# Optimization experiments

Hardware: AMD Instinct MI355X
Metric: run time of the kernel (lower is better)

## Reference

```python
import jax, jax.numpy as jnp
import numpy as np

IN_FEATURES = 4096
OUT_FEATURES = 2048
N_GROUPS = 16  # group size = IN_FEATURES // N_GROUPS = 256


def setup_inputs() -> dict:
    key = jax.random.key(0)
    k1, k2, k3, k4 = jax.random.split(key, 4)
    x = jax.random.normal(k1, (8, 64, IN_FEATURES), dtype=jnp.float32)
    # uint8 quantized weights, stored [out, in] as in the torch module
    qweight = jax.random.randint(k2, (OUT_FEATURES, IN_FEATURES), 0, 256).astype(jnp.uint8)
    # per-(out-channel, group) dequant scale and offset; scale ~ (max-min)/255 of rand weights
    qrange = jax.random.uniform(k3, (OUT_FEATURES, N_GROUPS), dtype=jnp.float32) * (2.0 / 255.0)
    qmin = -jax.random.uniform(k4, (OUT_FEATURES, N_GROUPS), dtype=jnp.float32)
    return {"x": x, "qweight": qweight, "qrange": qrange, "qmin": qmin}


def reference(x, qweight, qrange, qmin):
    # out[b,s,o] = sum_i x[b,s,i] * (q[o,i]*qrange[o,g(i)] + qmin[o,g(i)])
    B, S, IN = x.shape
    OUT, G = qrange.shape
    gs = IN // G
    xg = x.reshape(B, S, G, gs)                     # [B,S,G,gs]
    qg = qweight.reshape(OUT, G, gs).astype(x.dtype)  # [O,G,gs]
    # fused per-group dequant matmul: scale folded into the contraction
    out = jnp.einsum('bsgi,ogi,og->bso', xg, qg, qrange)
    # offset term: qmin[o,g] * sum_i_in_group x[b,s,i]
    out = out + jnp.einsum('bsg,og->bso', xg.sum(axis=-1), qmin)
    return out
```

## Files before the change

kernel.cpp:

```cpp
#include <hip/hip_runtime.h>
#include <hip/hip_bf16.h>


#define M_T 512
#define N_T 2048
#define K_T 4096
#define NGRP 16
#define BM 128
#define BN 128
#define BK 64
#define OUT_ELEMS (M_T * N_T)
#define W_ELEMS (N_T * K_T)
#define X_ELEMS (M_T * K_T)

typedef __attribute__((ext_vector_type(8))) short mfrag_t;
typedef __attribute__((ext_vector_type(8))) unsigned short u16x8;
typedef __attribute__((ext_vector_type(4))) float f32x4;

__device__ __forceinline__ unsigned short f2bf(float f) {
  union { __hip_bfloat16 h; unsigned short u; } c;
  c.h = __float2bfloat16(f);
  return c.u;
}

__global__ __launch_bounds__(256) void pack_kernel(
    const float* __restrict__ x, const int* __restrict__ qw,
    const float* __restrict__ qrange, const float* __restrict__ qmin,
    unsigned short* __restrict__ wsW, unsigned short* __restrict__ wsX) {
  const int bid = blockIdx.x;
  const int tid = threadIdx.x;
  if (bid < (W_ELEMS / 8) / 256) {
    const int gidx = bid * 256 + tid;
    const int o = gidx >> 9;
    const int k8 = gidx & 511;
    const int g = k8 >> 5;
    const float sc = qrange[o * NGRP + g];
    const float mn = qmin[o * NGRP + g];
    const int4* q = (const int4*)(qw + ((size_t)o << 12) + (k8 << 3));
    const int4 q0 = q[0], q1 = q[1];
    u16x8 p;
    p[0] = f2bf((float)q0.x * sc + mn); p[1] = f2bf((float)q0.y * sc + mn);
    p[2] = f2bf((float)q0.z * sc + mn); p[3] = f2bf((float)q0.w * sc + mn);
    p[4] = f2bf((float)q1.x * sc + mn); p[5] = f2bf((float)q1.y * sc + mn);
    p[6] = f2bf((float)q1.z * sc + mn); p[7] = f2bf((float)q1.w * sc + mn);
    *(u16x8*)(wsW + ((size_t)gidx << 3)) = p;
  } else {
    const int gidx = (bid - (W_ELEMS / 8) / 256) * 256 + tid;
    const float4* a = (const float4*)(x + ((size_t)gidx << 3));
    const float4 a0 = a[0], a1 = a[1];
    u16x8 p;
    p[0] = f2bf(a0.x); p[1] = f2bf(a0.y); p[2] = f2bf(a0.z); p[3] = f2bf(a0.w);
    p[4] = f2bf(a1.x); p[5] = f2bf(a1.y); p[6] = f2bf(a1.z); p[7] = f2bf(a1.w);
    *(u16x8*)(wsX + ((size_t)gidx << 3)) = p;
  }
}

template <int KSPLIT, bool XCDSWZ>
__global__ __launch_bounds__(256, 4) void dq_gemm_kernel(
    const unsigned short* __restrict__ wsX, const unsigned short* __restrict__ wsW,
    float* __restrict__ dst) {
  constexpr int KC = K_T / KSPLIT;
  constexpr int NTC = KC / BK;

  __shared__ __align__(16) unsigned short As[BM * BK];
  __shared__ __align__(16) unsigned short Bs[BN * BK];

  const int tid = threadIdx.x;
  int xt, yt, kc;
  if (XCDSWZ) {
    const int b = blockIdx.x;
    kc = b & 7;
    const int slot = b >> 3;
    xt = slot & 15;
    yt = slot >> 4;
  } else {
    const int b = blockIdx.x;
    xt = b & 15;
    yt = (b >> 4) & 3;
    kc = b >> 6;
  }
  const int n0 = xt * BN;
  const int m0 = yt * BM;
  const int kbase = kc * KC;

  const int lane = tid & 63;
  const int wv = tid >> 6;

  const int srow8 = lane >> 3;
  const int scol = (((lane & 7) ^ srow8) << 3);
  const unsigned short* gA = wsX + (size_t)(m0 + wv * 32 + srow8) * K_T + kbase + scol;
  const unsigned short* gB = wsW + (size_t)(n0 + wv * 32 + srow8) * K_T + kbase + scol;
  unsigned short* lA = &As[wv * 32 * BK];
  unsigned short* lB = &Bs[wv * 32 * BK];

#define STAGE(T)                                                              \
  do {                                                                        \
    const size_t o_ = (size_t)(T) * BK;                                       \
    _Pragma("unroll")                                                         \
    for (int c_ = 0; c_ < 4; ++c_) {                                          \
      __builtin_amdgcn_global_load_lds(                                       \
          (const __attribute__((address_space(1))) void*)(gA + o_ + (size_t)c_ * 8 * K_T), \
          (__attribute__((address_space(3))) void*)(lA + c_ * 8 * BK), 16, 0, 0); \
      __builtin_amdgcn_global_load_lds(                                       \
          (const __attribute__((address_space(1))) void*)(gB + o_ + (size_t)c_ * 8 * K_T), \
          (__attribute__((address_space(3))) void*)(lB + c_ * 8 * BK), 16, 0, 0); \
    }                                                                         \
  } while (0)

  const int wm = (wv >> 1) * 64;
  const int wn = (wv & 1) * 64;
  const int lr = lane & 15;
  const int lq = lane >> 4;
  const int rxl = lr & 7;

  f32x4 acc[4][4] = {};

  for (int t = 0; t < NTC; ++t) {
    if (t > 0) __syncthreads();
    STAGE(t);
    __syncthreads();

#pragma unroll
    for (int kk = 0; kk < 2; ++kk) {
      const int so = ((kk * 4 + lq) ^ rxl) << 3;
      mfrag_t bf[4];
#pragma unroll
      for (int fn = 0; fn < 4; ++fn)
        bf[fn] = *(const mfrag_t*)&Bs[(wn + fn * 16 + lr) * BK + so];
#pragma unroll
      for (int fm = 0; fm < 4; ++fm) {
        mfrag_t af = *(const mfrag_t*)&As[(wm + fm * 16 + lr) * BK + so];
#pragma unroll
        for (int fn = 0; fn < 4; ++fn)
          acc[fm][fn] = __builtin_amdgcn_mfma_f32_16x16x32_bf16(af, bf[fn], acc[fm][fn], 0, 0, 0);
      }
    }
  }
#undef STAGE

  float* base = dst + (size_t)kc * OUT_ELEMS;
#pragma unroll
  for (int fm = 0; fm < 4; ++fm) {
#pragma unroll
    for (int fn = 0; fn < 4; ++fn) {
      const int rr = m0 + wm + fm * 16 + lq * 4;
      const int c = n0 + wn + fn * 16 + lr;
      float* op = base + (size_t)rr * N_T + c;
      op[0 * (size_t)N_T] = acc[fm][fn][0];
      op[1 * (size_t)N_T] = acc[fm][fn][1];
      op[2 * (size_t)N_T] = acc[fm][fn][2];
      op[3 * (size_t)N_T] = acc[fm][fn][3];
    }
  }
}

template <int KSPLIT>
__global__ __launch_bounds__(256) void reduce_kernel(const float* __restrict__ ws,
                                                     float* __restrict__ out) {
  const int i4 = blockIdx.x * 256 + threadIdx.x;
  const size_t base = (size_t)i4 * 4;
  float4 a = *(const float4*)(ws + base);
#pragma unroll
  for (int s = 1; s < KSPLIT; ++s) {
    float4 b = *(const float4*)(ws + (size_t)s * OUT_ELEMS + base);
    a.x += b.x; a.y += b.y; a.z += b.z; a.w += b.w;
  }
  *(float4*)(out + base) = a;
}

__global__ void naive_kernel(const float* __restrict__ x, const int* __restrict__ qw,
                             const float* __restrict__ qrange, const float* __restrict__ qmin,
                             float* __restrict__ out) {
  const int idx = blockIdx.x * 256 + threadIdx.x;
  if (idx >= OUT_ELEMS) return;
  const int m = idx / N_T, n = idx % N_T;
  float s = 0.f;
  for (int g = 0; g < NGRP; ++g) {
    const float sc = qrange[n * NGRP + g], mn = qmin[n * NGRP + g];
    float d = 0.f, xs = 0.f;
    for (int k = g * 256; k < (g + 1) * 256; ++k) {
      d += x[(size_t)m * K_T + k] * (float)qw[(size_t)n * K_T + k];
      xs += x[(size_t)m * K_T + k];
    }
    s += d * sc + xs * mn;
  }
  out[idx] = s;
}

extern "C" void kernel_launch(void* const* d_in, const int* in_sizes, int n_in,
                              void* d_out, int out_size, void* d_ws, size_t ws_size,
                              hipStream_t stream) {
  const float* x = (const float*)d_in[0];
  const int* qw = (const int*)d_in[1];
  const float* qr = (const float*)d_in[2];
  const float* qm = (const float*)d_in[3];
  float* out = (float*)d_out;

  constexpr int KS = 8;
  unsigned short* wsW = (unsigned short*)d_ws;
  unsigned short* wsX = wsW + W_ELEMS;
  float* partials = (float*)(wsX + X_ELEMS);
  const size_t need = (size_t)W_ELEMS * 2 + (size_t)X_ELEMS * 2 +
                      (size_t)KS * OUT_ELEMS * sizeof(float);
  if (ws_size >= need) {
    const int packblk = (W_ELEMS / 8) / 256 + (X_ELEMS / 8) / 256;
    pack_kernel<<<packblk, 256, 0, stream>>>(x, qw, qr, qm, wsW, wsX);
    const int nblk = (N_T / BN) * (M_T / BM) * KS;
    dq_gemm_kernel<KS, true><<<nblk, dim3(256, 1, 1), 0, stream>>>(wsX, wsW, partials);
    reduce_kernel<KS><<<OUT_ELEMS / 4 / 256, 256, 0, stream>>>(partials, out);
  } else {
    naive_kernel<<<(OUT_ELEMS + 255) / 256, 256, 0, stream>>>(x, qw, qr, qm, out);
  }
}
```

Measured before the change: 36.48 us.

## Fuse weight dequant and activation bf16 conversion into a weight-resident split-K GEMM

Removes the separate pack kernel and the bf16 weight and activation workspaces. Each block dequantizes a 64x512 slice of the int weights straight into LDS, where it stays for the whole block. The block then streams fp32 activations for 256 rows, converting them to bf16 on the fly, and writes split-K partials. The aim is to avoid writing and re-reading the dequantized weights and activations through global memory, and to drop one kernel launch. In exchange, the activation staging is synchronous with no prefetch, uses smaller 128x64 output tiles per block, and needs about 80KB of LDS per block, which limits occupancy.

```diff
diff --git a/kernel.cpp b/kernel.cpp
--- a/kernel.cpp
+++ b/kernel.cpp
@@ -6,12 +6,11 @@
 #define N_T 2048
 #define K_T 4096
 #define NGRP 16
+#define KSPLIT 8
+#define KC 512
+#define BN 64
 #define BM 128
-#define BN 128
-#define BK 64
 #define OUT_ELEMS (M_T * N_T)
-#define W_ELEMS (N_T * K_T)
-#define X_ELEMS (M_T * K_T)
 
 typedef __attribute__((ext_vector_type(8))) short mfrag_t;
 typedef __attribute__((ext_vector_type(8))) unsigned short u16x8;
@@ -23,138 +22,124 @@
   return c.u;
 }
 
-__global__ __launch_bounds__(256) void pack_kernel(
+__global__ __launch_bounds__(512, 2) void wres_gemm_kernel(
     const float* __restrict__ x, const int* __restrict__ qw,
     const float* __restrict__ qrange, const float* __restrict__ qmin,
-    unsigned short* __restrict__ wsW, unsigned short* __restrict__ wsX) {
-  const int bid = blockIdx.x;
+    float* __restrict__ dst) {
+  __shared__ __align__(16) unsigned short WL[BN * KC];
+  __shared__ __align__(16) unsigned short XL[BM * 64];
+
+  const int b = blockIdx.x;
+  const int kc = b & 7;
+  const int slot = b >> 3;
+  const int xt = slot & 31;
+  const int mh = slot >> 5;
+  const int n0 = xt * BN;
+  const int kbase = kc * KC;
   const int tid = threadIdx.x;
-  if (bid < (W_ELEMS / 8) / 256) {
-    const int gidx = bid * 256 + tid;
-    const int o = gidx >> 9;
-    const int k8 = gidx & 511;
-    const int g = k8 >> 5;
-    const float sc = qrange[o * NGRP + g];
-    const float mn = qmin[o * NGRP + g];
-    const int4* q = (const int4*)(qw + ((size_t)o << 12) + (k8 << 3));
-    const int4 q0 = q[0], q1 = q[1];
-    u16x8 p;
-    p[0] = f2bf((float)q0.x * sc + mn); p[1] = f2bf((float)q0.y * sc + mn);
-    p[2] = f2bf((float)q0.z * sc + mn); p[3] = f2bf((float)q0.w * sc + mn);
-    p[4] = f2bf((float)q1.x * sc + mn); p[5] = f2bf((float)q1.y * sc + mn);
-    p[6] = f2bf((float)q1.z * sc + mn); p[7] = f2bf((float)q1.w * sc + mn);
-    *(u16x8*)(wsW + ((size_t)gidx << 3)) = p;
-  } else {
-    const int gidx = (bid - (W_ELEMS / 8) / 256) * 256 + tid;
-    const float4* a = (const float4*)(x + ((size_t)gidx << 3));
-    const float4 a0 = a[0], a1 = a[1];
-    u16x8 p;
-    p[0] = f2bf(a0.x); p[1] = f2bf(a0.y); p[2] = f2bf(a0.z); p[3] = f2bf(a0.w);
-    p[4] = f2bf(a1.x); p[5] = f2bf(a1.y); p[6] = f2bf(a1.z); p[7] = f2bf(a1.w);
-    *(u16x8*)(wsX + ((size_t)gidx << 3)) = p;
-  }
-}
-
-template <int KSPLIT, bool XCDSWZ>
-__global__ __launch_bounds__(256, 4) void dq_gemm_kernel(
-    const unsigned short* __restrict__ wsX, const unsigned short* __restrict__ wsW,
-    float* __restrict__ dst) {
-  constexpr int KC = K_T / KSPLIT;
-  constexpr int NTC = KC / BK;
-
-  __shared__ __align__(16) unsigned short As[BM * BK];
-  __shared__ __align__(16) unsigned short Bs[BN * BK];
-
-  const int tid = threadIdx.x;
-  int xt, yt, kc;
-  if (XCDSWZ) {
-    const int b = blockIdx.x;
-    kc = b & 7;
-    const int slot = b >> 3;
-    xt = slot & 15;
-    yt = slot >> 4;
-  } else {
-    const int b = blockIdx.x;
-    xt = b & 15;
-    yt = (b >> 4) & 3;
-    kc = b >> 6;
-  }
-  const int n0 = xt * BN;
-  const int m0 = yt * BM;
-  const int kbase = kc * KC;
-
   const int lane = tid & 63;
   const int wv = tid >> 6;
 
-  const int srow8 = lane >> 3;
-  const int scol = (((lane & 7) ^ srow8) << 3);
-  const unsigned short* gA = wsX + (size_t)(m0 + wv * 32 + srow8) * K_T + kbase + scol;
-  const unsigned short* gB = wsW + (size_t)(n0 + wv * 32 + srow8) * K_T + kbase + scol;
-  unsigned short* lA = &As[wv * 32 * BK];
-  unsigned short* lB = &Bs[wv * 32 * BK];
+  {
+    const int wrow = tid >> 3;
+    const int wc8 = tid & 7;
+    const int* qrow = qw + (size_t)(n0 + wrow) * K_T + kbase;
+    const float* qrp = qrange + (size_t)(n0 + wrow) * NGRP + kc * 2;
+    const float* qmp = qmin + (size_t)(n0 + wrow) * NGRP + kc * 2;
+    const float sc0 = qrp[0], mn0 = qmp[0];
+    const float sc1 = qrp[1], mn1 = qmp[1];
+    const int rx = wrow & 7;
+#pragma unroll
+    for (int c = 0; c < 4; ++c) {
+      const int col = wc8 * 16 + c * 128;
+      const int4* q4 = (const int4*)(qrow + col);
+      const int4 q0 = q4[0], q1 = q4[1], q2 = q4[2], q3 = q4[3];
+      const float sc = (c < 2) ? sc0 : sc1;
+      const float mn = (c < 2) ? mn0 : mn1;
+      u16x8 p0, p1;
+      p0[0] = f2bf((float)q0.x * sc + mn); p0[1] = f2bf((float)q0.y * sc + mn);
+      p0[2] = f2bf((float)q0.z * sc + mn); p0[3] = f2bf((float)q0.w * sc + mn);
+      p0[4] = f2bf((float)q1.x * sc + mn); p0[5] = f2bf((float)q1.y * sc + mn);
+      p0[6] = f2bf((float)q1.z * sc + mn); p0[7] = f2bf((float)q1.w * sc + mn);
+      p1[0] = f2bf((float)q2.x * sc + mn); p1[1] = f2bf((float)q2.y * sc + mn);
+      p1[2] = f2bf((float)q2.z * sc + mn); p1[3] = f2bf((float)q2.w * sc + mn);
+      p1[4] = f2bf((float)q3.x * sc + mn); p1[5] = f2bf((float)q3.y * sc + mn);
+      p1[6] = f2bf((float)q3.z * sc + mn); p1[7] = f2bf((float)q3.w * sc + mn);
+      const int s0 = (col >> 3) ^ rx;
+      const int s1 = ((col >> 3) + 1) ^ rx;
+      *(u16x8*)&WL[wrow * KC + s0 * 8] = p0;
+      *(u16x8*)&WL[wrow * KC + s1 * 8] = p1;
+    }
+  }
 
-#define STAGE(T)                                                              \
-  do {                                                                        \
-    const size_t o_ = (size_t)(T) * BK;                                       \
-    _Pragma("unroll")                                                         \
-    for (int c_ = 0; c_ < 4; ++c_) {                                          \
-      __builtin_amdgcn_global_load_lds(                                       \
-          (const __attribute__((address_space(1))) void*)(gA + o_ + (size_t)c_ * 8 * K_T), \
-          (__attribute__((address_space(3))) void*)(lA + c_ * 8 * BK), 16, 0, 0); \
-      __builtin_amdgcn_global_load_lds(                                       \
-          (const __attribute__((address_space(1))) void*)(gB + o_ + (size_t)c_ * 8 * K_T), \
-          (__attribute__((address_space(3))) void*)(lB + c_ * 8 * BK), 16, 0, 0); \
-    }                                                                         \
-  } while (0)
-
-  const int wm = (wv >> 1) * 64;
-  const int wn = (wv & 1) * 64;
+  const int wm = (wv >> 1) * 32;
+  const int wn = (wv & 1) * 32;
   const int lr = lane & 15;
   const int lq = lane >> 4;
-  const int rxl = lr & 7;
+  const int rxl = lr & 15 & 7;
 
-  f32x4 acc[4][4] = {};
+  const int xrow = tid >> 2;
+  const int xseg = tid & 3;
+  const int xrx = xrow & 7;
+  const int xs0 = (xseg * 2) ^ xrx;
+  const int xs1 = (xseg * 2 + 1) ^ xrx;
 
-  for (int t = 0; t < NTC; ++t) {
-    if (t > 0) __syncthreads();
-    STAGE(t);
-    __syncthreads();
+  float* pbase = dst + (size_t)kc * OUT_ELEMS;
 
 #pragma unroll
-    for (int kk = 0; kk < 2; ++kk) {
-      const int so = ((kk * 4 + lq) ^ rxl) << 3;
-      mfrag_t bf[4];
+  for (int mt = 0; mt < 2; ++mt) {
+    const int m0g = mh * 256 + mt * 128;
+    const float* xp = x + (size_t)(m0g + xrow) * K_T + kbase + xseg * 16;
+    f32x4 acc[2][2] = {};
+
+    for (int ks = 0; ks < 8; ++ks) {
+      if (mt > 0 || ks > 0) __syncthreads();
+
+      {
+        const float4* a4 = (const float4*)(xp + ks * 64);
+        const float4 a0 = a4[0], a1 = a4[1], a2 = a4[2], a3 = a4[3];
+        u16x8 p0, p1;
+        p0[0] = f2bf(a0.x); p0[1] = f2bf(a0.y); p0[2] = f2bf(a0.z); p0[3] = f2bf(a0.w);
+        p0[4] = f2bf(a1.x); p0[5] = f2bf(a1.y); p0[6] = f2bf(a1.z); p0[7] = f2bf(a1.w);
+        p1[0] = f2bf(a2.x); p1[1] = f2bf(a2.y); p1[2] = f2bf(a2.z); p1[3] = f2bf(a2.w);
+        p1[4] = f2bf(a3.x); p1[5] = f2bf(a3.y); p1[6] = f2bf(a3.z); p1[7] = f2bf(a3.w);
+        *(u16x8*)&XL[xrow * 64 + xs0 * 8] = p0;
+        *(u16x8*)&XL[xrow * 64 + xs1 * 8] = p1;
+      }
+      __syncthreads();
+
 #pragma unroll
-      for (int fn = 0; fn < 4; ++fn)
-        bf[fn] = *(const mfrag_t*)&Bs[(wn + fn * 16 + lr) * BK + so];
-#pragma unroll
-      for (int fm = 0; fm < 4; ++fm) {
-        mfrag_t af = *(const mfrag_t*)&As[(wm + fm * 16 + lr) * BK + so];
-#pragma unroll
-        for (int fn = 0; fn < 4; ++fn)
-          acc[fm][fn] = __builtin_amdgcn_mfma_f32_16x16x32_bf16(af, bf[fn], acc[fm][fn], 0, 0, 0);
+      for (int kk = 0; kk < 2; ++kk) {
+        const int sx = (kk * 4 + lq) ^ rxl;
+        const int sw = (ks * 8 + kk * 4 + lq) ^ rxl;
+        mfrag_t af[2], bf[2];
+        af[0] = *(const mfrag_t*)&XL[(wm + lr) * 64 + sx * 8];
+        af[1] = *(const mfrag_t*)&XL[(wm + 16 + lr) * 64 + sx * 8];
+        bf[0] = *(const mfrag_t*)&WL[(wn + lr) * KC + sw * 8];
+        bf[1] = *(const mfrag_t*)&WL[(wn + 16 + lr) * KC + sw * 8];
+        acc[0][0] = __builtin_amdgcn_mfma_f32_16x16x32_bf16(af[0], bf[0], acc[0][0], 0, 0, 0);
+        acc[0][1] = __builtin_amdgcn_mfma_f32_16x16x32_bf16(af[0], bf[1], acc[0][1], 0, 0, 0);
+        acc[1][0] = __builtin_amdgcn_mfma_f32_16x16x32_bf16(af[1], bf[0], acc[1][0], 0, 0, 0);
+        acc[1][1] = __builtin_amdgcn_mfma_f32_16x16x32_bf16(af[1], bf[1], acc[1][1], 0, 0, 0);
       }
     }
-  }
-#undef STAGE
 
-  float* base = dst + (size_t)kc * OUT_ELEMS;
 #pragma unroll
-  for (int fm = 0; fm < 4; ++fm) {
+    for (int fm = 0; fm < 2; ++fm) {
 #pragma unroll
-    for (int fn = 0; fn < 4; ++fn) {
-      const int rr = m0 + wm + fm * 16 + lq * 4;
-      const int c = n0 + wn + fn * 16 + lr;
-      float* op = base + (size_t)rr * N_T + c;
-      op[0 * (size_t)N_T] = acc[fm][fn][0];
-      op[1 * (size_t)N_T] = acc[fm][fn][1];
-      op[2 * (size_t)N_T] = acc[fm][fn][2];
-      op[3 * (size_t)N_T] = acc[fm][fn][3];
+      for (int fn = 0; fn < 2; ++fn) {
+        const int r0 = m0g + wm + fm * 16 + lq * 4;
+        const int c = n0 + wn + fn * 16 + lr;
+        float* op = pbase + (size_t)r0 * N_T + c;
+        op[0 * (size_t)N_T] = acc[fm][fn][0];
+        op[1 * (size_t)N_T] = acc[fm][fn][1];
+        op[2 * (size_t)N_T] = acc[fm][fn][2];
+        op[3 * (size_t)N_T] = acc[fm][fn][3];
+      }
     }
   }
 }
 
-template <int KSPLIT>
 __global__ __launch_bounds__(256) void reduce_kernel(const float* __restrict__ ws,
                                                      float* __restrict__ out) {
   const int i4 = blockIdx.x * 256 + threadIdx.x;
@@ -195,19 +180,12 @@
   const float* qr = (const float*)d_in[2];
   const float* qm = (const float*)d_in[3];
   float* out = (float*)d_out;
+  float* partials = (float*)d_ws;
 
-  constexpr int KS = 8;
-  unsigned short* wsW = (unsigned short*)d_ws;
-  unsigned short* wsX = wsW + W_ELEMS;
-  float* partials = (float*)(wsX + X_ELEMS);
-  const size_t need = (size_t)W_ELEMS * 2 + (size_t)X_ELEMS * 2 +
-                      (size_t)KS * OUT_ELEMS * sizeof(float);
+  const size_t need = (size_t)KSPLIT * OUT_ELEMS * sizeof(float);
   if (ws_size >= need) {
-    const int packblk = (W_ELEMS / 8) / 256 + (X_ELEMS / 8) / 256;
-    pack_kernel<<<packblk, 256, 0, stream>>>(x, qw, qr, qm, wsW, wsX);
-    const int nblk = (N_T / BN) * (M_T / BM) * KS;
-    dq_gemm_kernel<KS, true><<<nblk, dim3(256, 1, 1), 0, stream>>>(wsX, wsW, partials);
-    reduce_kernel<KS><<<OUT_ELEMS / 4 / 256, 256, 0, stream>>>(partials, out);
+    wres_gemm_kernel<<<512, dim3(512, 1, 1), 0, stream>>>(x, qw, qr, qm, partials);
+    reduce_kernel<<<OUT_ELEMS / 4 / 256, 256, 0, stream>>>(partials, out);
   } else {
     naive_kernel<<<(OUT_ELEMS + 255) / 256, 256, 0, stream>>>(x, qw, qr, qm, out);
   }
```

After: 43.93 us. 20.4% more time.
